# Optimization experiments

Measured on AMD Instinct MI355X. Metric: run time of the kernel, lower is better.

Reference implementation:

```python
import jax, jax.numpy as jnp
import numpy as np
import math

B, N, E, H = 2, 4096, 256, 8
HS = E // H  # head_size = 32


def setup_inputs() -> dict:
    key = jax.random.key(0)
    ks = jax.random.split(key, 8)
    s = 1.0 / math.sqrt(E)
    return {
        "node_features": jax.random.normal(ks[0], (B, N, E), dtype=jnp.float32),
        "adj": jax.random.randint(ks[1], (B, N, N), 0, 2).astype(jnp.bool_),
        "Wq": jax.random.normal(ks[2], (E, E), dtype=jnp.float32) * s,
        "bq": jax.random.normal(ks[3], (E,), dtype=jnp.float32) * s,
        "Wk": jax.random.normal(ks[4], (E, E), dtype=jnp.float32) * s,
        "bk": jax.random.normal(ks[5], (E,), dtype=jnp.float32) * s,
        "Wv": jax.random.normal(ks[6], (E, E), dtype=jnp.float32) * s,
        "bv": jax.random.normal(ks[7], (E,), dtype=jnp.float32) * s,
    }


def _split_heads(x):
    # (B, N, E) -> (B, H, N, HS)
    return x.reshape(B, N, H, HS).transpose(0, 2, 1, 3)


def reference(node_features, adj, Wq, bq, Wk, bk, Wv, bv):
    # nn.Linear: x @ W.T + b
    Q = _split_heads(node_features @ Wq.T + bq)
    K = _split_heads(node_features @ Wk.T + bk)
    V = _split_heads(node_features @ Wv.T + bv)
    scores = jnp.einsum("bhnd,bhmd->bhnm", Q, K) / math.sqrt(HS)
    scores = jnp.where(adj[:, None, :, :], scores, -jnp.inf)
    probs = jax.nn.softmax(scores, axis=-1)
    out = jnp.einsum("bhnm,bhmd->bhnd", probs, V)
    # (B, H, N, HS) -> (B, N, E); note: original forward does NOT apply W_out
    return out.transpose(0, 2, 1, 3).reshape(B, N, E)
```

## Files before the change

kernel.cpp:

```cpp
#include <hip/hip_runtime.h>

typedef __attribute__((ext_vector_type(8))) short short8;
typedef __attribute__((ext_vector_type(4))) float f32x4;
typedef __attribute__((ext_vector_type(4))) unsigned short u16x4;

constexpr int cB = 2, cN = 4096, cE = 256, cH = 8, cHS = 32;

__device__ __forceinline__ unsigned short f2bf(float f) {
    unsigned int u = __builtin_bit_cast(unsigned int, f);
    u = (u + 0x7FFFu + ((u >> 16) & 1u)) >> 16;
    return (unsigned short)u;
}

__device__ __forceinline__ unsigned int cvt_pk_bf16(float lo, float hi) {
    unsigned int r;
    asm("v_cvt_pk_bf16_f32 %0, %1, %2" : "=v"(r) : "v"(lo), "v"(hi));
    return r;
}

__global__ __launch_bounds__(256) void cvt_x_kernel(const float* __restrict__ x,
                                                    unsigned short* __restrict__ xb) {
    int t = blockIdx.x * 256 + threadIdx.x;
    f32x4 v = *((const f32x4*)x + t);
    u16x4 o = { f2bf(v[0]), f2bf(v[1]), f2bf(v[2]), f2bf(v[3]) };
    *((u16x4*)xb + t) = o;
}

__global__ __launch_bounds__(256) void cvt_w_kernel(const float* __restrict__ Wq,
                                                    const float* __restrict__ Wk,
                                                    const float* __restrict__ Wv,
                                                    unsigned short* __restrict__ wcb) {
    int t = blockIdx.x * 256 + threadIdx.x;
    int f = t * 4;
    int o = f >> 8, i = f & 255;
    const float* src = (o < 256) ? Wq : (o < 512 ? Wk : Wv);
    f32x4 v = *(const f32x4*)(src + (size_t)(o & 255) * 256 + i);
    u16x4 ov = { f2bf(v[0]), f2bf(v[1]), f2bf(v[2]), f2bf(v[3]) };
    *((u16x4*)wcb + t) = ov;
}

__global__ __launch_bounds__(256) void bitpack_kernel(const int* __restrict__ adj,
                                                      unsigned long long* __restrict__ mask) {
    int lane = threadIdx.x & 63;
    int wave = blockIdx.x * 4 + (threadIdx.x >> 6);
    const int nwaves = 2048 * 4;
    const int nwords = cB * cN * cN / 64;
    for (int w = wave; w < nwords; w += nwaves) {
        int v = adj[(size_t)w * 64 + lane];
        unsigned long long bal = __ballot(v != 0);
        if (lane == 0) mask[w] = bal;
    }
}

__global__ __launch_bounds__(256) void qkv_proj_kernel(const unsigned short* __restrict__ xb,
                                                       const unsigned short* __restrict__ wcb,
                                                       const float* __restrict__ bq,
                                                       const float* __restrict__ bk,
                                                       const float* __restrict__ bv,
                                                       unsigned short* __restrict__ Qb,
                                                       unsigned short* __restrict__ Kb,
                                                       unsigned short* __restrict__ Vt) {
    const int wv = threadIdx.x >> 6, lane = threadIdx.x & 63;
    const int col = lane & 15, grp = lane >> 4;
    const int rowbase = blockIdx.x * 64 + wv * 16;
    const int colbase = blockIdx.y * 64;
    const float CE = 1.4426950408889634f * 0.17677669529663687f;
    f32x4 acc[4] = {};
    for (int kk = 0; kk < 8; ++kk) {
        short8 a = *(const short8*)(xb + (size_t)(rowbase + col) * 256 + kk * 32 + grp * 8);
        #pragma unroll
        for (int c = 0; c < 4; ++c) {
            short8 bf = *(const short8*)(wcb + (size_t)(colbase + c * 16 + col) * 256 + kk * 32 + grp * 8);
            acc[c] = __builtin_amdgcn_mfma_f32_16x16x32_bf16(a, bf, acc[c], 0, 0, 0);
        }
    }
    #pragma unroll
    for (int c = 0; c < 4; ++c) {
        const int o = colbase + c * 16 + col;
        const int sel = o >> 8, oo = o & 255;
        const float bias = (sel == 0 ? bq : sel == 1 ? bk : bv)[oo];
        const int h = oo >> 5, hs = oo & 31;
        const int R0 = rowbase + grp * 4;
        const int b = R0 >> 12, n0 = R0 & 4095;
        if (sel == 0) {
            #pragma unroll
            for (int r = 0; r < 4; ++r)
                Qb[(size_t)((b * cH + h) * cN + n0 + r) * cHS + hs] = f2bf((acc[c][r] + bias) * CE);
        } else if (sel == 1) {
            #pragma unroll
            for (int r = 0; r < 4; ++r)
                Kb[(size_t)((b * cH + h) * cN + n0 + r) * cHS + hs] = f2bf(acc[c][r] + bias);
        } else {
            unsigned short* vrow = Vt + (size_t)((b * cH + h) * cHS + hs) * cN;
            #pragma unroll
            for (int r = 0; r < 4; ++r) {
                const int n = n0 + r;
                const int pos = (n & ~31) + 2 * (n & 15) + ((n >> 4) & 1);
                vrow[pos] = f2bf(acc[c][r] + bias);
            }
        }
    }
}

__global__ __launch_bounds__(256, 5) void attn_kernel(const unsigned short* __restrict__ Qb,
                                                      const unsigned short* __restrict__ Kb,
                                                      const unsigned short* __restrict__ Vt,
                                                      const unsigned int* __restrict__ mask32,
                                                      float* __restrict__ out) {
    __shared__ float comb[4][64][24];
    const int wv = threadIdx.x >> 6, lane = threadIdx.x & 63;
    const int col = lane & 15, grp = lane >> 4;
    int bid = blockIdx.x;
    bid = (bid & 7) * 256 + (bid >> 3);
    const int qt = bid & 127, h = (bid >> 7) & 7, b = bid >> 10;
    const int qbase = qt * 32;
    const unsigned short* Qh = Qb + (size_t)(b * cH + h) * cN * cHS;
    const unsigned short* Kh = Kb + (size_t)(b * cH + h) * cN * cHS;
    const unsigned short* Vh = Vt + (size_t)(b * cH + h) * cHS * cN;
    const unsigned int* mrow = mask32 + (size_t)(b * cN + qbase) * 128;
    unsigned int* pw = (unsigned int*)&comb[0][0][0] + wv * 640;

    const short8 aq0 = *(const short8*)(Qh + (size_t)(qbase + col) * cHS + grp * 8);
    const short8 aq1 = *(const short8*)(Qh + (size_t)(qbase + 16 + col) * cHS + grp * 8);

    f32x4 acc[2][2] = {};
    f32x4 lacc[2] = {};
    const f32x4 z4 = {0.f, 0.f, 0.f, 0.f};
    const short8 ones = { 0x3F80, 0x3F80, 0x3F80, 0x3F80, 0x3F80, 0x3F80, 0x3F80, 0x3F80 };

    const int ktEnd = wv * 32 + 32;
    #pragma unroll 1
    for (int kt = wv * 32; kt < ktEnd; ++kt) {
        const int kbase = kt * 32;
        const short8 k0 = *(const short8*)(Kh + (size_t)(kbase + col) * cHS + grp * 8);
        const short8 k1 = *(const short8*)(Kh + (size_t)(kbase + 16 + col) * cHS + grp * 8);
        const short8 v0 = *(const short8*)(Vh + (size_t)col * cN + kbase + grp * 8);
        const short8 v1 = *(const short8*)(Vh + (size_t)(16 + col) * cN + kbase + grp * 8);

        f32x4 s[2][2];
        s[0][0] = __builtin_amdgcn_mfma_f32_16x16x32_bf16(aq0, k0, z4, 0, 0, 0);
        s[0][1] = __builtin_amdgcn_mfma_f32_16x16x32_bf16(aq0, k1, z4, 0, 0, 0);
        s[1][0] = __builtin_amdgcn_mfma_f32_16x16x32_bf16(aq1, k0, z4, 0, 0, 0);
        s[1][1] = __builtin_amdgcn_mfma_f32_16x16x32_bf16(aq1, k1, z4, 0, 0, 0);

        #pragma unroll
        for (int qs = 0; qs < 2; ++qs) {
            #pragma unroll
            for (int r = 0; r < 4; ++r) {
                const unsigned int w32 = mrow[(size_t)(qs * 16 + grp * 4 + r) * 128 + kt];
                const float e0 = __builtin_exp2f(s[qs][0][r]);
                const float e1 = __builtin_exp2f(s[qs][1][r]);
                const unsigned int msk = ((w32 >> col) & 0x00010001u) * 0xFFFFu;
                pw[qs * 320 + (grp * 4 + r) * 20 + col] = cvt_pk_bf16(e0, e1) & msk;
            }
        }
        #pragma unroll
        for (int qs = 0; qs < 2; ++qs) {
            const short8 pa = *(const short8*)(pw + qs * 320 + col * 20 + grp * 4);
            acc[qs][0] = __builtin_amdgcn_mfma_f32_16x16x32_bf16(pa, v0, acc[qs][0], 0, 0, 0);
            acc[qs][1] = __builtin_amdgcn_mfma_f32_16x16x32_bf16(pa, v1, acc[qs][1], 0, 0, 0);
            lacc[qs]   = __builtin_amdgcn_mfma_f32_16x16x32_bf16(pa, ones, lacc[qs], 0, 0, 0);
        }
    }

    __syncthreads();
    float* me = &comb[wv][lane][0];
    *(f32x4*)(me +  0) = acc[0][0];
    *(f32x4*)(me +  4) = acc[0][1];
    *(f32x4*)(me +  8) = acc[1][0];
    *(f32x4*)(me + 12) = acc[1][1];
    *(f32x4*)(me + 16) = lacc[0];
    *(f32x4*)(me + 20) = lacc[1];
    __syncthreads();

    const int sg = wv, qs = sg >> 1, half = sg & 1;
    const int grp2 = lane >> 4, col2 = lane & 15;
    f32x4 a = {0.f, 0.f, 0.f, 0.f};
    f32x4 l = {0.f, 0.f, 0.f, 0.f};
    #pragma unroll
    for (int w = 0; w < 4; ++w) {
        a += *(const f32x4*)&comb[w][lane][sg * 4];
        l += *(const f32x4*)&comb[w][lane][16 + qs * 4];
    }
    const int row0 = qbase + qs * 16 + grp2 * 4;
    #pragma unroll
    for (int j = 0; j < 4; ++j) {
        out[(size_t)(b * cN + row0 + j) * cE + h * 32 + half * 16 + col2] = a[j] / l[j];
    }
}

extern "C" void kernel_launch(void* const* d_in, const int* in_sizes, int n_in,
                              void* d_out, int out_size, void* d_ws, size_t ws_size,
                              hipStream_t stream) {
    const float* x   = (const float*)d_in[0];
    const int*   adj = (const int*)d_in[1];
    const float* Wq  = (const float*)d_in[2];
    const float* bq  = (const float*)d_in[3];
    const float* Wk  = (const float*)d_in[4];
    const float* bk  = (const float*)d_in[5];
    const float* Wv  = (const float*)d_in[6];
    const float* bv  = (const float*)d_in[7];
    float* out = (float*)d_out;

    char* ws = (char*)d_ws;
    unsigned short* Xb  = (unsigned short*)(ws);
    unsigned short* Wcb = (unsigned short*)(ws + (4ull << 20));
    unsigned short* Qb  = (unsigned short*)(ws + (5ull << 20));
    unsigned short* Kb  = (unsigned short*)(ws + (9ull << 20));
    unsigned short* Vt  = (unsigned short*)(ws + (13ull << 20));
    unsigned long long* mask64 = (unsigned long long*)(ws + (17ull << 20));

    cvt_x_kernel<<<dim3(2048), dim3(256), 0, stream>>>(x, Xb);
    cvt_w_kernel<<<dim3(192), dim3(256), 0, stream>>>(Wq, Wk, Wv, Wcb);
    bitpack_kernel<<<dim3(2048), dim3(256), 0, stream>>>(adj, mask64);
    qkv_proj_kernel<<<dim3(128, 12), dim3(256), 0, stream>>>(Xb, Wcb, bq, bk, bv, Qb, Kb, Vt);
    attn_kernel<<<dim3(2048), dim3(256), 0, stream>>>(Qb, Kb, Vt, (const unsigned int*)mask64, out);
}
```

Measured before the change: 180.9 us.

## Software-prefetch K/V/mask tiles and process two query tiles per attention block

The attention kernel now loads the next K, V and mask tiles into registers while computing the current one, so global-load latency overlaps with MFMA and exp work. Each block handles two query tiles in sequence, which halves the grid and adds a trailing barrier between tiles. The occupancy hint drops from 5 to 4 blocks per CU to make room for the extra prefetch registers. The cost is more register pressure and lower occupancy, plus a serial second tile per block.

```diff
diff --git a/kernel.cpp b/kernel.cpp
--- a/kernel.cpp
+++ b/kernel.cpp
@@ -102,7 +102,7 @@
     }
 }
 
-__global__ __launch_bounds__(256, 5) void attn_kernel(const unsigned short* __restrict__ Qb,
+__global__ __launch_bounds__(256, 4) void attn_kernel(const unsigned short* __restrict__ Qb,
                                                       const unsigned short* __restrict__ Kb,
                                                       const unsigned short* __restrict__ Vt,
                                                       const unsigned int* __restrict__ mask32,
@@ -111,81 +111,103 @@
     const int wv = threadIdx.x >> 6, lane = threadIdx.x & 63;
     const int col = lane & 15, grp = lane >> 4;
     int bid = blockIdx.x;
-    bid = (bid & 7) * 256 + (bid >> 3);
-    const int qt = bid & 127, h = (bid >> 7) & 7, b = bid >> 10;
-    const int qbase = qt * 32;
+    bid = (bid & 7) * 128 + (bid >> 3);
+    const int qt0 = bid & 63, h = (bid >> 6) & 7, b = bid >> 9;
     const unsigned short* Qh = Qb + (size_t)(b * cH + h) * cN * cHS;
     const unsigned short* Kh = Kb + (size_t)(b * cH + h) * cN * cHS;
     const unsigned short* Vh = Vt + (size_t)(b * cH + h) * cHS * cN;
-    const unsigned int* mrow = mask32 + (size_t)(b * cN + qbase) * 128;
     unsigned int* pw = (unsigned int*)&comb[0][0][0] + wv * 640;
-
-    const short8 aq0 = *(const short8*)(Qh + (size_t)(qbase + col) * cHS + grp * 8);
-    const short8 aq1 = *(const short8*)(Qh + (size_t)(qbase + 16 + col) * cHS + grp * 8);
-
-    f32x4 acc[2][2] = {};
-    f32x4 lacc[2] = {};
     const f32x4 z4 = {0.f, 0.f, 0.f, 0.f};
     const short8 ones = { 0x3F80, 0x3F80, 0x3F80, 0x3F80, 0x3F80, 0x3F80, 0x3F80, 0x3F80 };
-
-    const int ktEnd = wv * 32 + 32;
+    const int kt0 = wv * 32;
+
     #pragma unroll 1
-    for (int kt = wv * 32; kt < ktEnd; ++kt) {
-        const int kbase = kt * 32;
-        const short8 k0 = *(const short8*)(Kh + (size_t)(kbase + col) * cHS + grp * 8);
-        const short8 k1 = *(const short8*)(Kh + (size_t)(kbase + 16 + col) * cHS + grp * 8);
-        const short8 v0 = *(const short8*)(Vh + (size_t)col * cN + kbase + grp * 8);
-        const short8 v1 = *(const short8*)(Vh + (size_t)(16 + col) * cN + kbase + grp * 8);
-
-        f32x4 s[2][2];
-        s[0][0] = __builtin_amdgcn_mfma_f32_16x16x32_bf16(aq0, k0, z4, 0, 0, 0);
-        s[0][1] = __builtin_amdgcn_mfma_f32_16x16x32_bf16(aq0, k1, z4, 0, 0, 0);
-        s[1][0] = __builtin_amdgcn_mfma_f32_16x16x32_bf16(aq1, k0, z4, 0, 0, 0);
-        s[1][1] = __builtin_amdgcn_mfma_f32_16x16x32_bf16(aq1, k1, z4, 0, 0, 0);
-
-        #pragma unroll
-        for (int qs = 0; qs < 2; ++qs) {
-            #pragma unroll
-            for (int r = 0; r < 4; ++r) {
-                const unsigned int w32 = mrow[(size_t)(qs * 16 + grp * 4 + r) * 128 + kt];
-                const float e0 = __builtin_exp2f(s[qs][0][r]);
-                const float e1 = __builtin_exp2f(s[qs][1][r]);
-                const unsigned int msk = ((w32 >> col) & 0x00010001u) * 0xFFFFu;
-                pw[qs * 320 + (grp * 4 + r) * 20 + col] = cvt_pk_bf16(e0, e1) & msk;
-            }
-        }
-        #pragma unroll
-        for (int qs = 0; qs < 2; ++qs) {
-            const short8 pa = *(const short8*)(pw + qs * 320 + col * 20 + grp * 4);
-            acc[qs][0] = __builtin_amdgcn_mfma_f32_16x16x32_bf16(pa, v0, acc[qs][0], 0, 0, 0);
-            acc[qs][1] = __builtin_amdgcn_mfma_f32_16x16x32_bf16(pa, v1, acc[qs][1], 0, 0, 0);
-            lacc[qs]   = __builtin_amdgcn_mfma_f32_16x16x32_bf16(pa, ones, lacc[qs], 0, 0, 0);
-        }
-    }
-
-    __syncthreads();
-    float* me = &comb[wv][lane][0];
-    *(f32x4*)(me +  0) = acc[0][0];
-    *(f32x4*)(me +  4) = acc[0][1];
-    *(f32x4*)(me +  8) = acc[1][0];
-    *(f32x4*)(me + 12) = acc[1][1];
-    *(f32x4*)(me + 16) = lacc[0];
-    *(f32x4*)(me + 20) = lacc[1];
-    __syncthreads();
-
-    const int sg = wv, qs = sg >> 1, half = sg & 1;
-    const int grp2 = lane >> 4, col2 = lane & 15;
-    f32x4 a = {0.f, 0.f, 0.f, 0.f};
-    f32x4 l = {0.f, 0.f, 0.f, 0.f};
-    #pragma unroll
-    for (int w = 0; w < 4; ++w) {
-        a += *(const f32x4*)&comb[w][lane][sg * 4];
-        l += *(const f32x4*)&comb[w][lane][16 + qs * 4];
-    }
-    const int row0 = qbase + qs * 16 + grp2 * 4;
-    #pragma unroll
-    for (int j = 0; j < 4; ++j) {
-        out[(size_t)(b * cN + row0 + j) * cE + h * 32 + half * 16 + col2] = a[j] / l[j];
+    for (int tk = 0; tk < 2; ++tk) {
+        const int qbase = (qt0 + tk * 64) * 32;
+        const unsigned int* mrow = mask32 + (size_t)(b * cN + qbase) * 128;
+
+        const short8 aq0 = *(const short8*)(Qh + (size_t)(qbase + col) * cHS + grp * 8);
+        const short8 aq1 = *(const short8*)(Qh + (size_t)(qbase + 16 + col) * cHS + grp * 8);
+
+        f32x4 acc[2][2] = {};
+        f32x4 lacc[2] = {};
+
+        short8 ck0 = *(const short8*)(Kh + (size_t)(kt0 * 32 + col) * cHS + grp * 8);
+        short8 ck1 = *(const short8*)(Kh + (size_t)(kt0 * 32 + 16 + col) * cHS + grp * 8);
+        short8 cv0 = *(const short8*)(Vh + (size_t)col * cN + kt0 * 32 + grp * 8);
+        short8 cv1 = *(const short8*)(Vh + (size_t)(16 + col) * cN + kt0 * 32 + grp * 8);
+        unsigned int cm[8];
+        #pragma unroll
+        for (int i = 0; i < 8; ++i)
+            cm[i] = mrow[(size_t)((i >> 2) * 16 + grp * 4 + (i & 3)) * 128 + kt0];
+
+        #pragma unroll 2
+        for (int kt = kt0; kt < kt0 + 32; ++kt) {
+            const short8 k0 = ck0, k1 = ck1, v0 = cv0, v1 = cv1;
+            unsigned int m8[8];
+            #pragma unroll
+            for (int i = 0; i < 8; ++i) m8[i] = cm[i];
+            if (kt < kt0 + 31) {
+                const int kb = (kt + 1) * 32;
+                ck0 = *(const short8*)(Kh + (size_t)(kb + col) * cHS + grp * 8);
+                ck1 = *(const short8*)(Kh + (size_t)(kb + 16 + col) * cHS + grp * 8);
+                cv0 = *(const short8*)(Vh + (size_t)col * cN + kb + grp * 8);
+                cv1 = *(const short8*)(Vh + (size_t)(16 + col) * cN + kb + grp * 8);
+                #pragma unroll
+                for (int i = 0; i < 8; ++i)
+                    cm[i] = mrow[(size_t)((i >> 2) * 16 + grp * 4 + (i & 3)) * 128 + kt + 1];
+            }
+
+            f32x4 s[2][2];
+            s[0][0] = __builtin_amdgcn_mfma_f32_16x16x32_bf16(aq0, k0, z4, 0, 0, 0);
+            s[0][1] = __builtin_amdgcn_mfma_f32_16x16x32_bf16(aq0, k1, z4, 0, 0, 0);
+            s[1][0] = __builtin_amdgcn_mfma_f32_16x16x32_bf16(aq1, k0, z4, 0, 0, 0);
+            s[1][1] = __builtin_amdgcn_mfma_f32_16x16x32_bf16(aq1, k1, z4, 0, 0, 0);
+
+            #pragma unroll
+            for (int qs = 0; qs < 2; ++qs) {
+                #pragma unroll
+                for (int r = 0; r < 4; ++r) {
+                    const unsigned int w32 = m8[qs * 4 + r];
+                    const float e0 = __builtin_exp2f(s[qs][0][r]);
+                    const float e1 = __builtin_exp2f(s[qs][1][r]);
+                    const unsigned int msk = ((w32 >> col) & 0x00010001u) * 0xFFFFu;
+                    pw[qs * 320 + (grp * 4 + r) * 20 + col] = cvt_pk_bf16(e0, e1) & msk;
+                }
+            }
+            #pragma unroll
+            for (int qs = 0; qs < 2; ++qs) {
+                const short8 pa = *(const short8*)(pw + qs * 320 + col * 20 + grp * 4);
+                acc[qs][0] = __builtin_amdgcn_mfma_f32_16x16x32_bf16(pa, v0, acc[qs][0], 0, 0, 0);
+                acc[qs][1] = __builtin_amdgcn_mfma_f32_16x16x32_bf16(pa, v1, acc[qs][1], 0, 0, 0);
+                lacc[qs]   = __builtin_amdgcn_mfma_f32_16x16x32_bf16(pa, ones, lacc[qs], 0, 0, 0);
+            }
+        }
+
+        __syncthreads();
+        float* me = &comb[wv][lane][0];
+        *(f32x4*)(me +  0) = acc[0][0];
+        *(f32x4*)(me +  4) = acc[0][1];
+        *(f32x4*)(me +  8) = acc[1][0];
+        *(f32x4*)(me + 12) = acc[1][1];
+        *(f32x4*)(me + 16) = lacc[0];
+        *(f32x4*)(me + 20) = lacc[1];
+        __syncthreads();
+
+        const int sg = wv, qs2 = sg >> 1, half = sg & 1;
+        f32x4 a = {0.f, 0.f, 0.f, 0.f};
+        f32x4 l = {0.f, 0.f, 0.f, 0.f};
+        #pragma unroll
+        for (int w = 0; w < 4; ++w) {
+            a += *(const f32x4*)&comb[w][lane][sg * 4];
+            l += *(const f32x4*)&comb[w][lane][16 + qs2 * 4];
+        }
+        const int row0 = qbase + qs2 * 16 + grp * 4;
+        #pragma unroll
+        for (int j = 0; j < 4; ++j) {
+            out[(size_t)(b * cN + row0 + j) * cE + h * 32 + half * 16 + col] = a[j] / l[j];
+        }
+        __syncthreads();
     }
 }
 
@@ -214,5 +236,5 @@
     cvt_w_kernel<<<dim3(192), dim3(256), 0, stream>>>(Wq, Wk, Wv, Wcb);
     bitpack_kernel<<<dim3(2048), dim3(256), 0, stream>>>(adj, mask64);
     qkv_proj_kernel<<<dim3(128, 12), dim3(256), 0, stream>>>(Xb, Wcb, bq, bk, bv, Qb, Kb, Vt);
-    attn_kernel<<<dim3(2048), dim3(256), 0, stream>>>(Qb, Kb, Vt, (const unsigned int*)mask64, out);
-}
+    attn_kernel<<<dim3(1024), dim3(256), 0, stream>>>(Qb, Kb, Vt, (const unsigned int*)mask64, out);
+}
```

After: 212.5 us. +17.5%, slower.
